# Performance work log

Hardware: AMD Instinct MI355X
Metric: run time of the kernel (lower is better)

## Reference

```python
import jax, jax.numpy as jnp
import numpy as np

N = 50000   # nodes
E = 800000  # edges
F = 128     # input features
W = 128     # hidden width
K = 5       # Chebyshev order


def setup_inputs() -> dict:
    key = jax.random.key(0)
    ks = jax.random.split(key, 12)
    x = jax.random.normal(ks[0], (N, F), jnp.float32)
    edge_index = jax.random.randint(ks[1], (2, E), 0, N, jnp.int32)
    def p(i, shape):
        return jax.random.normal(ks[i], shape, jnp.float32) * 0.05
    return {
        'x': x,
        'edge_index': edge_index,
        'W0': p(2, (K, F, W)), 'b0': p(3, (W,)),
        'W1': p(4, (K, W, W)), 'b1': p(5, (W,)),
        'W2': p(6, (K, W, W)), 'b2': p(7, (W,)),
        'Wl': p(8, (W, 1)),   'bl': p(9, (1,)),
    }


def _norm(edge_index):
    # PyG ChebConv norm with lambda_max=2.0, sym normalization:
    # Lhat = 2/lambda_max * (I - D^-1/2 A D^-1/2) - I  ->  diag 0, offdiag -d_r*d_c
    src, dst = edge_index[0], edge_index[1]
    ew = (src != dst).astype(jnp.float32)  # remove self loops
    deg = jax.ops.segment_sum(ew, src, num_segments=N)
    dinv = jnp.where(deg > 0, jax.lax.rsqrt(jnp.maximum(deg, 1.0)), 0.0)
    w = -ew * dinv[src] * dinv[dst]
    return src, dst, w


def _cheb_conv(h, Wk, b, src, dst, w):
    # Tx_0 = h; Tx_1 = Lhat h; Tx_k = 2 Lhat Tx_{k-1} - Tx_{k-2}
    def matvec(v):
        # gather from src, weight, scatter-add to dst: [E, C] message tensor
        return jax.ops.segment_sum(w[:, None] * v[src], dst, num_segments=N)
    Tx0 = h
    out = Tx0 @ Wk[0]
    Tx1 = matvec(Tx0)
    out = out + Tx1 @ Wk[1]
    for k in range(2, Wk.shape[0]):
        Tx2 = 2.0 * matvec(Tx1) - Tx0
        out = out + Tx2 @ Wk[k]
        Tx0, Tx1 = Tx1, Tx2
    return out + b


def reference(x, edge_index, W0, b0, W1, b1, W2, b2, Wl, bl):
    src, dst, w = _norm(edge_index)
    h = jax.nn.relu(_cheb_conv(x, W0, b0, src, dst, w))  # dropout = identity (eval)
    h = jax.nn.relu(_cheb_conv(h, W1, b1, src, dst, w))
    h = _cheb_conv(h, W2, b2, src, dst, w)
    return h @ Wl + bl  # [N, 1]
```

## Files before the change

kernel.cpp:

```cpp
#include <hip/hip_runtime.h>
#include <hip/hip_bf16.h>
#include <stdint.h>

#define N_NODES 50000
#define N_EDGES 800000
#define FEAT 128
#define CAP 64
#define NCVT 1600000
#define NTRW 163840
#define NPRE (NCVT + NTRW + N_EDGES)

typedef __attribute__((ext_vector_type(4))) float floatx4;
typedef __attribute__((ext_vector_type(8))) _Float16 half8;
typedef __attribute__((ext_vector_type(4))) _Float16 half4;

__device__ __forceinline__ float bf2f(unsigned short u) {
  union { unsigned u; float f; } v; v.u = ((unsigned)u) << 16; return v.f;
}
__device__ __forceinline__ unsigned short f2bf(float f) {
  union { float f; unsigned u; } v; v.f = f;
  unsigned r = v.u + 0x7fffu + ((v.u >> 16) & 1u);
  return (unsigned short)(r >> 16);
}
__device__ __forceinline__ unsigned pack_edge(float w, int s) {
  _Float16 h = (_Float16)w;
  unsigned short hb = __builtin_bit_cast(unsigned short, h);
  return ((unsigned)s << 16) | (unsigned)hb;
}
__device__ __forceinline__ float edge_w(unsigned e) {
  unsigned short hb = (unsigned short)(e & 0xFFFFu);
  return (float)__builtin_bit_cast(_Float16, hb);
}
__device__ __forceinline__ int edge_src(unsigned e) { return (int)(e >> 16); }

__global__ void k_pre1(const unsigned short* __restrict__ x,
                       const void* b0, const void* b1, const void* b2,
                       const void* wl, const void* bl,
                       float* __restrict__ pf, int* __restrict__ flag) {
  __shared__ int cnt_s;
  __shared__ int fl_s;
  int tid = threadIdx.x;
  if (tid == 0) cnt_s = 0;
  __syncthreads();
  int big = 0;
  for (int i = tid; i < 4096; i += 256) {
    unsigned short u = x[2 * i];
    int e = (u >> 7) & 0xFF;
    if (e >= 0xE0) big++;
  }
  atomicAdd(&cnt_s, big);
  __syncthreads();
  if (tid == 0) { fl_s = (cnt_s > 16) ? 1 : 0; flag[0] = fl_s; }
  __syncthreads();
  int fl = fl_s;
  for (int i = tid; i < 513; i += 256) {
    const void* src; int off;
    if (i < 128)      { src = b0; off = i; }
    else if (i < 256) { src = b1; off = i - 128; }
    else if (i < 384) { src = b2; off = i - 256; }
    else if (i < 512) { src = wl; off = i - 384; }
    else              { src = bl; off = 0; }
    pf[i] = fl ? ((const float*)src)[off] : bf2f(((const unsigned short*)src)[off]);
  }
}

__global__ void k_prev(const void* __restrict__ w2, float* __restrict__ pf,
                       const int* __restrict__ flag) {
  int d = blockIdx.x * 256 + threadIdx.x;
  if (d > 640) return;
  int fl = flag[0];
  if (d < 640) {
    int k = d >> 7, f = d & 127;
    float s = 0.f;
    const int base = (k << 14) + (f << 7);
    if (fl) {
      const float* w = (const float*)w2 + base;
#pragma unroll 8
      for (int i = 0; i < 128; ++i) s += w[i] * pf[384 + i];
    } else {
      const unsigned short* w = (const unsigned short*)w2 + base;
#pragma unroll 8
      for (int i = 0; i < 128; ++i) s += bf2f(w[i]) * pf[384 + i];
    }
    pf[520 + d] = s;
  } else {
    float s = 0.f;
    for (int i = 0; i < 128; ++i) s += pf[256 + i] * pf[384 + i];
    pf[1160] = s + pf[512];
  }
}

__global__ void k_pre2(const void* __restrict__ xp,
                       const void* __restrict__ w0, const void* __restrict__ w1,
                       const int* __restrict__ esrc, const int* __restrict__ edst,
                       _Float16* __restrict__ t0,
                       unsigned char* __restrict__ q0, float* __restrict__ s0,
                       _Float16* __restrict__ wt,
                       int* __restrict__ deg,
                       const int* __restrict__ flag) {
  int i = blockIdx.x * blockDim.x + threadIdx.x;
  int fl = flag[0];
  if (i < NCVT) {
    float4 o;
    if (fl) {
      o = ((const float4*)xp)[i];
    } else {
      ushort4 v = ((const ushort4*)xp)[i];
      o.x = bf2f(v.x); o.y = bf2f(v.y); o.z = bf2f(v.z); o.w = bf2f(v.w);
    }
    half4 h;
    h[0] = (_Float16)o.x; h[1] = (_Float16)o.y; h[2] = (_Float16)o.z; h[3] = (_Float16)o.w;
    ((half4*)t0)[i] = h;
    float mx = fmaxf(fmaxf(fabsf(o.x), fabsf(o.y)), fmaxf(fabsf(o.z), fabsf(o.w)));
#pragma unroll
    for (int d = 1; d < 32; d <<= 1) mx = fmaxf(mx, __shfl_xor(mx, d));
    float inv = mx > 0.f ? 127.f / mx : 0.f;
    int qa = (int)rintf(o.x * inv) + 128;
    int qb = (int)rintf(o.y * inv) + 128;
    int qc = (int)rintf(o.z * inv) + 128;
    int qd = (int)rintf(o.w * inv) + 128;
    ((unsigned*)q0)[i] = (unsigned)qa | ((unsigned)qb << 8) | ((unsigned)qc << 16) | ((unsigned)qd << 24);
    if ((i & 31) == 0) s0[i >> 5] = mx > 0.f ? mx / 127.f : 0.f;
  } else if (i < NCVT + NTRW) {
    int tid = i - NCVT;
    int li = tid >> 14;
    int r = tid & 16383;
    int n = r >> 7, kk = r & 127;
    int l = li / 5, k = li - l * 5;
    const void* w = (l == 0) ? w0 : w1;
    int idx = k * 16384 + kk * 128 + n;
    float v = fl ? ((const float*)w)[idx] : bf2f(((const unsigned short*)w)[idx]);
    wt[tid] = (_Float16)v;
  } else {
    int e = i - (NCVT + NTRW);
    if (e >= N_EDGES) return;
    int s = esrc[e], d = edst[e];
    if (s != d) atomicAdd(&deg[s], 1);
  }
}

__global__ void k_fill(const int* __restrict__ src, const int* __restrict__ dst,
                       const int* __restrict__ deg,
                       int* __restrict__ cnt, unsigned* __restrict__ edata) {
  int e = blockIdx.x * blockDim.x + threadIdx.x;
  if (e >= N_EDGES) return;
  int s = src[e], d = dst[e];
  if (s == d) return;
  int ds = deg[s], dd = deg[d];
  float w = (ds > 0 && dd > 0) ? -rsqrtf((float)ds) * rsqrtf((float)dd) : 0.f;
  int pos = atomicAdd(&cnt[d], 1);
  if (pos < CAP) edata[(d << 6) + pos] = pack_edge(w, s);
}

__global__ __launch_bounds__(256) void k_spmv(const unsigned* __restrict__ edata,
                                              const int* __restrict__ cnt,
                                              const unsigned char* __restrict__ Q,
                                              const float* __restrict__ S,
                                              const _Float16* __restrict__ Z,
                                              _Float16* __restrict__ Y,
                                              unsigned char* __restrict__ Qo,
                                              float* __restrict__ So,
                                              float alpha, int hasZ, int wshadow) {
  int wave = threadIdx.x >> 6, lane = threadIdx.x & 63;
  int q = lane >> 4, l16 = lane & 15;
  int node = blockIdx.x * 16 + wave * 4 + q;
  if (node >= N_NODES) return;
  int n_e = cnt[node]; if (n_e > CAP) n_e = CAP;
  int base = node << 6;

  float acc[8];
#pragma unroll
  for (int f = 0; f < 8; ++f) acc[f] = 0.f;
  float wsum = 0.f;

  unsigned e0 = (0 < n_e) ? edata[base + 0] : 0u;
  unsigned e1 = (1 < n_e) ? edata[base + 1] : 0u;
  unsigned e2 = (2 < n_e) ? edata[base + 2] : 0u;
  unsigned e3 = (3 < n_e) ? edata[base + 3] : 0u;
  unsigned e4 = (4 < n_e) ? edata[base + 4] : 0u;
  unsigned e5 = (5 < n_e) ? edata[base + 5] : 0u;
  unsigned e6 = (6 < n_e) ? edata[base + 6] : 0u;
  unsigned e7 = (7 < n_e) ? edata[base + 7] : 0u;
  uint2 r0 = ((const uint2*)(Q + (size_t)edge_src(e0) * FEAT))[l16];
  uint2 r1 = ((const uint2*)(Q + (size_t)edge_src(e1) * FEAT))[l16];
  uint2 r2 = ((const uint2*)(Q + (size_t)edge_src(e2) * FEAT))[l16];
  uint2 r3 = ((const uint2*)(Q + (size_t)edge_src(e3) * FEAT))[l16];
  float s0 = S[edge_src(e0)], s1 = S[edge_src(e1)], s2 = S[edge_src(e2)], s3 = S[edge_src(e3)];

  for (int j = 0; j < n_e; j += 4) {
    float ws0 = edge_w(e0) * s0, ws1 = edge_w(e1) * s1;
    float ws2 = edge_w(e2) * s2, ws3 = edge_w(e3) * s3;
    uint2 c0 = r0, c1 = r1, c2 = r2, c3 = r3;
    e0 = e4; e1 = e5; e2 = e6; e3 = e7;
    e4 = (j + 8 < n_e) ? edata[base + j + 8] : 0u;
    e5 = (j + 9 < n_e) ? edata[base + j + 9] : 0u;
    e6 = (j + 10 < n_e) ? edata[base + j + 10] : 0u;
    e7 = (j + 11 < n_e) ? edata[base + j + 11] : 0u;
    r0 = ((const uint2*)(Q + (size_t)edge_src(e0) * FEAT))[l16];
    r1 = ((const uint2*)(Q + (size_t)edge_src(e1) * FEAT))[l16];
    r2 = ((const uint2*)(Q + (size_t)edge_src(e2) * FEAT))[l16];
    r3 = ((const uint2*)(Q + (size_t)edge_src(e3) * FEAT))[l16];
    s0 = S[edge_src(e0)]; s1 = S[edge_src(e1)]; s2 = S[edge_src(e2)]; s3 = S[edge_src(e3)];
#define DEC8(c, w)                                                        \
    acc[0] = fmaf(w, (float)(c.x & 0xFFu), acc[0]);                       \
    acc[1] = fmaf(w, (float)((c.x >> 8) & 0xFFu), acc[1]);                \
    acc[2] = fmaf(w, (float)((c.x >> 16) & 0xFFu), acc[2]);               \
    acc[3] = fmaf(w, (float)(c.x >> 24), acc[3]);                         \
    acc[4] = fmaf(w, (float)(c.y & 0xFFu), acc[4]);                       \
    acc[5] = fmaf(w, (float)((c.y >> 8) & 0xFFu), acc[5]);                \
    acc[6] = fmaf(w, (float)((c.y >> 16) & 0xFFu), acc[6]);               \
    acc[7] = fmaf(w, (float)(c.y >> 24), acc[7]);
    DEC8(c0, ws0) DEC8(c1, ws1) DEC8(c2, ws2) DEC8(c3, ws3)
#undef DEC8
    wsum += (ws0 + ws1) + (ws2 + ws3);
  }
  float rx[8];
  float b128 = 128.f * wsum;
  if (hasZ) {
    half8 z = ((const half8*)(Z + (size_t)node * FEAT))[l16];
#pragma unroll
    for (int f = 0; f < 8; ++f) rx[f] = fmaf(alpha, acc[f] - b128, -(float)z[f]);
  } else {
#pragma unroll
    for (int f = 0; f < 8; ++f) rx[f] = alpha * (acc[f] - b128);
  }
  half8 res;
#pragma unroll
  for (int f = 0; f < 8; ++f) res[f] = (_Float16)rx[f];
  ((half8*)(Y + (size_t)node * FEAT))[l16] = res;
  if (wshadow) {
    float mx = 0.f;
#pragma unroll
    for (int f = 0; f < 8; ++f) mx = fmaxf(mx, fabsf(rx[f]));
#pragma unroll
    for (int o = 1; o < 16; o <<= 1) mx = fmaxf(mx, __shfl_xor(mx, o));
    float inv = mx > 0.f ? 127.f / mx : 0.f;
    int qb[8];
#pragma unroll
    for (int f = 0; f < 8; ++f) qb[f] = (int)rintf(rx[f] * inv) + 128;
    uint2 p;
    p.x = (unsigned)qb[0] | ((unsigned)qb[1] << 8) | ((unsigned)qb[2] << 16) | ((unsigned)qb[3] << 24);
    p.y = (unsigned)qb[4] | ((unsigned)qb[5] << 8) | ((unsigned)qb[6] << 16) | ((unsigned)qb[7] << 24);
    ((uint2*)(Qo + (size_t)node * FEAT))[l16] = p;
    if (l16 == 0) So[node] = mx > 0.f ? mx / 127.f : 0.f;
  }
}

__global__ __launch_bounds__(256) void k_smv(const unsigned* __restrict__ edata,
                                             const int* __restrict__ cnt,
                                             const float* __restrict__ h,
                                             const float* __restrict__ b,
                                             const float* __restrict__ bprev,
                                             float cL, float* __restrict__ y,
                                             int is_out, void* __restrict__ outp,
                                             const int* __restrict__ flag,
                                             const float* __restrict__ cptr) {
  int wave = threadIdx.x >> 6, lane = threadIdx.x & 63;
  int q = lane >> 4, l16 = lane & 15;
  int node = blockIdx.x * 16 + wave * 4 + q;
  if (node >= N_NODES) return;
  int n_e = cnt[node]; if (n_e > CAP) n_e = CAP;
  int base = node << 6;
  float s = 0.f;
  for (int j = l16; j < n_e; j += 16) {
    unsigned e = edata[base + j];
    s = fmaf(edge_w(e), b[edge_src(e)], s);
  }
#pragma unroll
  for (int o = 1; o < 16; o <<= 1) s += __shfl_xor(s, o);
  if (l16 == 0) {
    float r = fmaf(cL, s, h[node]) - (bprev ? bprev[node] : 0.f);
    if (!is_out) {
      y[node] = r;
    } else {
      r += cptr[0];
      if (flag[0]) ((float*)outp)[node] = r;
      else ((unsigned short*)outp)[node] = f2bf(r);
    }
  }
}

__global__ __launch_bounds__(256) void k_gemm(const _Float16* __restrict__ t0, const _Float16* __restrict__ t1,
                                              const _Float16* __restrict__ t2, const _Float16* __restrict__ t3,
                                              const _Float16* __restrict__ t4,
                                              const _Float16* __restrict__ wt,
                                              const float* __restrict__ bias,
                                              _Float16* __restrict__ dst, int mode,
                                              const float* __restrict__ v0,
                                              float* __restrict__ hout,
                                              unsigned char* __restrict__ q8,
                                              float* __restrict__ sc) {
  __shared__ _Float16 lb[128 * 136];
  const _Float16* tp[5] = {t0, t1, t2, t3, t4};
  int tid = threadIdx.x, wave = tid >> 6, lane = tid & 63;
  int quad = lane >> 4, l16 = lane & 15;
  int m0 = blockIdx.x * 128;
  floatx4 acc[2][8];
#pragma unroll
  for (int s = 0; s < 2; ++s)
#pragma unroll
    for (int j = 0; j < 8; ++j) acc[s][j] = (floatx4){0.f, 0.f, 0.f, 0.f};
  int arow[2];
  bool aval[2];
#pragma unroll
  for (int s = 0; s < 2; ++s) {
    arow[s] = m0 + wave * 32 + s * 16 + l16;
    aval[s] = arow[s] < N_NODES;
  }

#pragma unroll
  for (int k = 0; k < 5; ++k) {
    __syncthreads();
    {
      int n = tid >> 1, half = tid & 1;
      const uint4* sp = (const uint4*)(wt + k * 16384 + n * 128 + half * 64);
      uint4* dq = (uint4*)(lb + n * 136 + half * 64);
#pragma unroll
      for (int i = 0; i < 8; ++i) dq[i] = sp[i];
    }
    __syncthreads();
    const _Float16* A = tp[k];
#pragma unroll
    for (int ki = 0; ki < 4; ++ki) {
      half8 af[2];
#pragma unroll
      for (int s = 0; s < 2; ++s) {
        if (aval[s]) {
          af[s] = *((const half8*)(A + (size_t)arow[s] * FEAT + ki * 32 + quad * 8));
        } else {
#pragma unroll
          for (int i = 0; i < 8; ++i) af[s][i] = (_Float16)0.f;
        }
      }
#pragma unroll
      for (int j = 0; j < 8; ++j) {
        half8 bf = *((const half8*)(lb + (j * 16 + l16) * 136 + ki * 32 + quad * 8));
        acc[0][j] = __builtin_amdgcn_mfma_f32_16x16x32_f16(af[0], bf, acc[0][j], 0, 0, 0);
        acc[1][j] = __builtin_amdgcn_mfma_f32_16x16x32_f16(af[1], bf, acc[1][j], 0, 0, 0);
      }
    }
  }
#pragma unroll
  for (int s = 0; s < 2; ++s) {
    int rbase = m0 + wave * 32 + s * 16 + quad * 4;
    if (mode == 0) {
      float mx[4] = {0.f, 0.f, 0.f, 0.f};
#pragma unroll
      for (int j = 0; j < 8; ++j) {
        int col = j * 16 + l16;
        float b = bias[col];
#pragma unroll
        for (int r = 0; r < 4; ++r) {
          int m = rbase + r;
          float v = fmaxf(acc[s][j][r] + b, 0.f);
          if (m < N_NODES) dst[(size_t)m * FEAT + col] = (_Float16)v;
          mx[r] = fmaxf(mx[r], v);
        }
      }
#pragma unroll
      for (int o = 1; o < 16; o <<= 1) {
#pragma unroll
        for (int r = 0; r < 4; ++r) mx[r] = fmaxf(mx[r], __shfl_xor(mx[r], o));
      }
      float inv[4];
#pragma unroll
      for (int r = 0; r < 4; ++r) inv[r] = mx[r] > 0.f ? 127.f / mx[r] : 0.f;
      if (l16 == 0) {
#pragma unroll
        for (int r = 0; r < 4; ++r) {
          int m = rbase + r;
          if (m < N_NODES) sc[m] = mx[r] > 0.f ? mx[r] / 127.f : 0.f;
        }
      }
#pragma unroll
      for (int j = 0; j < 8; ++j) {
        int col = j * 16 + l16;
        float b = bias[col];
#pragma unroll
        for (int r = 0; r < 4; ++r) {
          int m = rbase + r;
          if (m < N_NODES) {
            float v = fmaxf(acc[s][j][r] + b, 0.f);
            int qv = (int)rintf(v * inv[r]) + 128;
            q8[(size_t)m * FEAT + col] = (unsigned char)qv;
          }
        }
      }
    } else {
      float p[5][4];
#pragma unroll
      for (int k = 0; k < 5; ++k)
#pragma unroll
        for (int r = 0; r < 4; ++r) p[k][r] = 0.f;
#pragma unroll
      for (int j = 0; j < 8; ++j) {
        int col = j * 16 + l16;
        float b = bias[col];
        float vv[5];
#pragma unroll
        for (int k = 0; k < 5; ++k) vv[k] = v0[k * 128 + col];
#pragma unroll
        for (int r = 0; r < 4; ++r) {
          float val = fmaxf(acc[s][j][r] + b, 0.f);
#pragma unroll
          for (int k = 0; k < 5; ++k) p[k][r] = fmaf(val, vv[k], p[k][r]);
        }
      }
#pragma unroll
      for (int o = 1; o < 16; o <<= 1) {
#pragma unroll
        for (int k = 0; k < 5; ++k)
#pragma unroll
          for (int r = 0; r < 4; ++r) p[k][r] += __shfl_xor(p[k][r], o);
      }
      if (l16 == 0) {
#pragma unroll
        for (int r = 0; r < 4; ++r) {
          int m = rbase + r;
          if (m < N_NODES) {
#pragma unroll
            for (int k = 0; k < 5; ++k) hout[k * N_NODES + m] = p[k][r];
          }
        }
      }
    }
  }
}

extern "C" void kernel_launch(void* const* d_in, const int* in_sizes, int n_in,
                              void* d_out, int out_size, void* d_ws, size_t ws_size,
                              hipStream_t stream) {
  const void* x  = d_in[0];
  const int* ei  = (const int*)d_in[1];
  const void* w0 = d_in[2];
  const void* b0 = d_in[3];
  const void* w1 = d_in[4];
  const void* b1 = d_in[5];
  const void* w2 = d_in[6];
  const void* b2 = d_in[7];
  const void* wl = d_in[8];
  const void* bl = d_in[9];
  const int* src = ei;
  const int* dst = ei + N_EDGES;

  char* ws = (char*)d_ws;
  size_t off = 0;
  auto alloc = [&](size_t bytes) -> char* {
    char* p = ws + off;
    off += (bytes + 255) & ~(size_t)255;
    return p;
  };
  _Float16* T[5];
  for (int i = 0; i < 5; ++i) T[i] = (_Float16*)alloc(sizeof(_Float16) * N_NODES * FEAT);
  unsigned char* Q[5];
  for (int i = 0; i < 5; ++i) Q[i] = (unsigned char*)alloc((size_t)N_NODES * FEAT);
  float* S[5];
  for (int i = 0; i < 5; ++i) S[i] = (float*)alloc(sizeof(float) * N_NODES);
  unsigned* edata = (unsigned*)alloc(sizeof(unsigned) * N_NODES * CAP);
  int* cnt = (int*)alloc(sizeof(int) * N_NODES * 2);
  int* deg = cnt + N_NODES;
  _Float16* wt = (_Float16*)alloc(sizeof(_Float16) * NTRW);
  float* pf = (float*)alloc(sizeof(float) * 1536);
  float* hbuf = (float*)alloc(sizeof(float) * 5 * N_NODES);
  float* bbuf = (float*)alloc(sizeof(float) * 3 * N_NODES);
  int* flag = (int*)alloc(sizeof(int));

  hipMemsetAsync(cnt, 0, sizeof(int) * N_NODES * 2, stream);
  k_pre1<<<1, 256, 0, stream>>>((const unsigned short*)x, b0, b1, b2, wl, bl, pf, flag);
  k_prev<<<3, 256, 0, stream>>>(w2, pf, flag);
  k_pre2<<<(NPRE + 255) / 256, 256, 0, stream>>>(x, w0, w1, src, dst, T[0], Q[0], S[0], wt, deg, flag);
  k_fill<<<(N_EDGES + 255) / 256, 256, 0, stream>>>(src, dst, deg, cnt, edata);

  int nblk_spmv = (N_NODES + 15) / 16;
  int nblk_gemm = (N_NODES + 127) / 128;
  const float* v = pf + 520;
  const float* cc = pf + 1160;

  for (int l = 0; l < 2; ++l) {
    k_spmv<<<nblk_spmv, 256, 0, stream>>>(edata, cnt, Q[0], S[0], nullptr, T[1], Q[1], S[1], 1.f, 0, 1);
    k_spmv<<<nblk_spmv, 256, 0, stream>>>(edata, cnt, Q[1], S[1], T[0], T[2], Q[2], S[2], 2.f, 1, 1);
    k_spmv<<<nblk_spmv, 256, 0, stream>>>(edata, cnt, Q[2], S[2], T[1], T[3], Q[3], S[3], 2.f, 1, 1);
    k_spmv<<<nblk_spmv, 256, 0, stream>>>(edata, cnt, Q[3], S[3], T[2], T[4], nullptr, nullptr, 2.f, 1, 0);
    k_gemm<<<nblk_gemm, 256, 0, stream>>>(T[0], T[1], T[2], T[3], T[4],
                                          wt + l * 5 * 16384, pf + l * 128, T[0],
                                          l, v, hbuf, Q[0], S[0]);
  }
  float* h0 = hbuf;
  float* h1 = hbuf + N_NODES;
  float* h2 = hbuf + 2 * N_NODES;
  float* h3 = hbuf + 3 * N_NODES;
  float* h4 = hbuf + 4 * N_NODES;
  float* b3 = bbuf;
  float* b2c = bbuf + N_NODES;
  float* b1c = bbuf + 2 * N_NODES;
  k_smv<<<nblk_spmv, 256, 0, stream>>>(edata, cnt, h3, h4, nullptr, 2.f, b3, 0, nullptr, flag, nullptr);
  k_smv<<<nblk_spmv, 256, 0, stream>>>(edata, cnt, h2, b3, h4, 2.f, b2c, 0, nullptr, flag, nullptr);
  k_smv<<<nblk_spmv, 256, 0, stream>>>(edata, cnt, h1, b2c, b3, 2.f, b1c, 0, nullptr, flag, nullptr);
  k_smv<<<nblk_spmv, 256, 0, stream>>>(edata, cnt, h0, b1c, b2c, 1.f, nullptr, 1, d_out, flag, cc);
}
```

Before: 449.9 us.

## Fuse edge fill and weight precompute into preprocessing; store 16-bit edge sources

Folds the k_fill and k_prev kernels into k_pre2, which removes two launches and one pass over the edge list. Degree counting and CSR-style bucket filling now happen in the same edge pass. Edge weights are no longer stored: the bucket keeps only a 16-bit source index, and the spmv/smv kernels rebuild the normalisation from deg (rsqrt of the source degree per edge, times the destination scale at the end). The input streams in preprocessing also switch to nontemporal loads and stores. The cost of this is an extra random gather of deg per edge in every propagation kernel, in exchange for half-size edge data.

```diff
diff --git a/kernel.cpp b/kernel.cpp
--- a/kernel.cpp
+++ b/kernel.cpp
@@ -8,11 +8,13 @@
 #define CAP 64
 #define NCVT 1600000
 #define NTRW 163840
-#define NPRE (NCVT + NTRW + N_EDGES)
+#define NPREV 768
+#define NPRE2 (NCVT + NTRW + N_EDGES + NPREV)
 
 typedef __attribute__((ext_vector_type(4))) float floatx4;
 typedef __attribute__((ext_vector_type(8))) _Float16 half8;
 typedef __attribute__((ext_vector_type(4))) _Float16 half4;
+typedef __attribute__((ext_vector_type(4))) unsigned short ushortx4;
 
 __device__ __forceinline__ float bf2f(unsigned short u) {
   union { unsigned u; float f; } v; v.u = ((unsigned)u) << 16; return v.f;
@@ -22,16 +24,6 @@
   unsigned r = v.u + 0x7fffu + ((v.u >> 16) & 1u);
   return (unsigned short)(r >> 16);
 }
-__device__ __forceinline__ unsigned pack_edge(float w, int s) {
-  _Float16 h = (_Float16)w;
-  unsigned short hb = __builtin_bit_cast(unsigned short, h);
-  return ((unsigned)s << 16) | (unsigned)hb;
-}
-__device__ __forceinline__ float edge_w(unsigned e) {
-  unsigned short hb = (unsigned short)(e & 0xFFFFu);
-  return (float)__builtin_bit_cast(_Float16, hb);
-}
-__device__ __forceinline__ int edge_src(unsigned e) { return (int)(e >> 16); }
 
 __global__ void k_pre1(const unsigned short* __restrict__ x,
                        const void* b0, const void* b1, const void* b2,
@@ -64,53 +56,30 @@
   }
 }
 
-__global__ void k_prev(const void* __restrict__ w2, float* __restrict__ pf,
-                       const int* __restrict__ flag) {
-  int d = blockIdx.x * 256 + threadIdx.x;
-  if (d > 640) return;
-  int fl = flag[0];
-  if (d < 640) {
-    int k = d >> 7, f = d & 127;
-    float s = 0.f;
-    const int base = (k << 14) + (f << 7);
-    if (fl) {
-      const float* w = (const float*)w2 + base;
-#pragma unroll 8
-      for (int i = 0; i < 128; ++i) s += w[i] * pf[384 + i];
-    } else {
-      const unsigned short* w = (const unsigned short*)w2 + base;
-#pragma unroll 8
-      for (int i = 0; i < 128; ++i) s += bf2f(w[i]) * pf[384 + i];
-    }
-    pf[520 + d] = s;
-  } else {
-    float s = 0.f;
-    for (int i = 0; i < 128; ++i) s += pf[256 + i] * pf[384 + i];
-    pf[1160] = s + pf[512];
-  }
-}
-
 __global__ void k_pre2(const void* __restrict__ xp,
                        const void* __restrict__ w0, const void* __restrict__ w1,
+                       const void* __restrict__ w2,
                        const int* __restrict__ esrc, const int* __restrict__ edst,
                        _Float16* __restrict__ t0,
                        unsigned char* __restrict__ q0, float* __restrict__ s0,
                        _Float16* __restrict__ wt,
-                       int* __restrict__ deg,
+                       int* __restrict__ deg, int* __restrict__ cnt,
+                       unsigned short* __restrict__ edata,
+                       float* __restrict__ pf,
                        const int* __restrict__ flag) {
   int i = blockIdx.x * blockDim.x + threadIdx.x;
-  int fl = flag[0];
   if (i < NCVT) {
-    float4 o;
+    int fl = flag[0];
+    floatx4 o;
     if (fl) {
-      o = ((const float4*)xp)[i];
+      o = __builtin_nontemporal_load((const floatx4*)xp + i);
     } else {
-      ushort4 v = ((const ushort4*)xp)[i];
+      ushortx4 v = __builtin_nontemporal_load((const ushortx4*)xp + i);
       o.x = bf2f(v.x); o.y = bf2f(v.y); o.z = bf2f(v.z); o.w = bf2f(v.w);
     }
     half4 h;
     h[0] = (_Float16)o.x; h[1] = (_Float16)o.y; h[2] = (_Float16)o.z; h[3] = (_Float16)o.w;
-    ((half4*)t0)[i] = h;
+    __builtin_nontemporal_store(h, (half4*)t0 + i);
     float mx = fmaxf(fmaxf(fabsf(o.x), fabsf(o.y)), fmaxf(fabsf(o.z), fabsf(o.w)));
 #pragma unroll
     for (int d = 1; d < 32; d <<= 1) mx = fmaxf(mx, __shfl_xor(mx, d));
@@ -119,9 +88,11 @@
     int qb = (int)rintf(o.y * inv) + 128;
     int qc = (int)rintf(o.z * inv) + 128;
     int qd = (int)rintf(o.w * inv) + 128;
-    ((unsigned*)q0)[i] = (unsigned)qa | ((unsigned)qb << 8) | ((unsigned)qc << 16) | ((unsigned)qd << 24);
+    unsigned pk = (unsigned)qa | ((unsigned)qb << 8) | ((unsigned)qc << 16) | ((unsigned)qd << 24);
+    __builtin_nontemporal_store(pk, (unsigned*)q0 + i);
     if ((i & 31) == 0) s0[i >> 5] = mx > 0.f ? mx / 127.f : 0.f;
   } else if (i < NCVT + NTRW) {
+    int fl = flag[0];
     int tid = i - NCVT;
     int li = tid >> 14;
     int r = tid & 16383;
@@ -131,29 +102,44 @@
     int idx = k * 16384 + kk * 128 + n;
     float v = fl ? ((const float*)w)[idx] : bf2f(((const unsigned short*)w)[idx]);
     wt[tid] = (_Float16)v;
+  } else if (i < NCVT + NTRW + N_EDGES) {
+    int e = i - (NCVT + NTRW);
+    int s = __builtin_nontemporal_load(esrc + e);
+    int d = __builtin_nontemporal_load(edst + e);
+    if (s == d) return;
+    atomicAdd(&deg[s], 1);
+    int pos = atomicAdd(&cnt[d], 1);
+    if (pos < CAP) edata[((size_t)d << 6) + pos] = (unsigned short)s;
   } else {
-    int e = i - (NCVT + NTRW);
-    if (e >= N_EDGES) return;
-    int s = esrc[e], d = edst[e];
-    if (s != d) atomicAdd(&deg[s], 1);
-  }
-}
-
-__global__ void k_fill(const int* __restrict__ src, const int* __restrict__ dst,
-                       const int* __restrict__ deg,
-                       int* __restrict__ cnt, unsigned* __restrict__ edata) {
-  int e = blockIdx.x * blockDim.x + threadIdx.x;
-  if (e >= N_EDGES) return;
-  int s = src[e], d = dst[e];
-  if (s == d) return;
-  int ds = deg[s], dd = deg[d];
-  float w = (ds > 0 && dd > 0) ? -rsqrtf((float)ds) * rsqrtf((float)dd) : 0.f;
-  int pos = atomicAdd(&cnt[d], 1);
-  if (pos < CAP) edata[(d << 6) + pos] = pack_edge(w, s);
-}
-
-__global__ __launch_bounds__(256) void k_spmv(const unsigned* __restrict__ edata,
+    int t = i - (NCVT + NTRW + N_EDGES);
+    if (t > 640) return;
+    int fl = flag[0];
+    if (t < 640) {
+      int k = t >> 7, f = t & 127;
+      float s = 0.f;
+      const int base = (k << 14) + (f << 7);
+      if (fl) {
+        const float* w = (const float*)w2 + base;
+#pragma unroll 8
+        for (int q = 0; q < 128; ++q) s += w[q] * pf[384 + q];
+      } else {
+        const unsigned short* w = (const unsigned short*)w2 + base;
+#pragma unroll 8
+        for (int q = 0; q < 128; ++q) s += bf2f(w[q]) * pf[384 + q];
+      }
+      pf[520 + t] = s;
+    } else {
+      float s = 0.f;
+      for (int q = 0; q < 128; ++q) s += pf[256 + q] * pf[384 + q];
+      pf[1160] = s + pf[512];
+    }
+  }
+}
+
+
+__global__ __launch_bounds__(256) void k_spmv(const unsigned short* __restrict__ edata,
                                               const int* __restrict__ cnt,
+                                              const int* __restrict__ deg,
                                               const unsigned char* __restrict__ Q,
                                               const float* __restrict__ S,
                                               const _Float16* __restrict__ Z,
@@ -166,41 +152,40 @@
   int node = blockIdx.x * 16 + wave * 4 + q;
   if (node >= N_NODES) return;
   int n_e = cnt[node]; if (n_e > CAP) n_e = CAP;
-  int base = node << 6;
+  const unsigned short* ed = edata + ((size_t)node << 6);
 
   float acc[8];
 #pragma unroll
   for (int f = 0; f < 8; ++f) acc[f] = 0.f;
   float wsum = 0.f;
 
-  unsigned e0 = (0 < n_e) ? edata[base + 0] : 0u;
-  unsigned e1 = (1 < n_e) ? edata[base + 1] : 0u;
-  unsigned e2 = (2 < n_e) ? edata[base + 2] : 0u;
-  unsigned e3 = (3 < n_e) ? edata[base + 3] : 0u;
-  unsigned e4 = (4 < n_e) ? edata[base + 4] : 0u;
-  unsigned e5 = (5 < n_e) ? edata[base + 5] : 0u;
-  unsigned e6 = (6 < n_e) ? edata[base + 6] : 0u;
-  unsigned e7 = (7 < n_e) ? edata[base + 7] : 0u;
-  uint2 r0 = ((const uint2*)(Q + (size_t)edge_src(e0) * FEAT))[l16];
-  uint2 r1 = ((const uint2*)(Q + (size_t)edge_src(e1) * FEAT))[l16];
-  uint2 r2 = ((const uint2*)(Q + (size_t)edge_src(e2) * FEAT))[l16];
-  uint2 r3 = ((const uint2*)(Q + (size_t)edge_src(e3) * FEAT))[l16];
-  float s0 = S[edge_src(e0)], s1 = S[edge_src(e1)], s2 = S[edge_src(e2)], s3 = S[edge_src(e3)];
+#define LOADE(t, sv, wv)                                  \
+  if ((t) < n_e) {                                        \
+    int _s = (int)ed[(t)];                                \
+    sv = _s;                                              \
+    wv = rsqrtf((float)deg[_s]) * S[_s];                  \
+  } else { sv = 0; wv = 0.f; }
+
+  int s0, s1, s2, s3, s4, s5, s6, s7;
+  float w0, w1, w2, w3, w4, w5, w6, w7;
+  LOADE(0, s0, w0) LOADE(1, s1, w1) LOADE(2, s2, w2) LOADE(3, s3, w3)
+  LOADE(4, s4, w4) LOADE(5, s5, w5) LOADE(6, s6, w6) LOADE(7, s7, w7)
+  uint2 r0 = ((const uint2*)(Q + (size_t)s0 * FEAT))[l16];
+  uint2 r1 = ((const uint2*)(Q + (size_t)s1 * FEAT))[l16];
+  uint2 r2 = ((const uint2*)(Q + (size_t)s2 * FEAT))[l16];
+  uint2 r3 = ((const uint2*)(Q + (size_t)s3 * FEAT))[l16];
 
   for (int j = 0; j < n_e; j += 4) {
-    float ws0 = edge_w(e0) * s0, ws1 = edge_w(e1) * s1;
-    float ws2 = edge_w(e2) * s2, ws3 = edge_w(e3) * s3;
+    float ws0 = w0, ws1 = w1, ws2 = w2, ws3 = w3;
     uint2 c0 = r0, c1 = r1, c2 = r2, c3 = r3;
-    e0 = e4; e1 = e5; e2 = e6; e3 = e7;
-    e4 = (j + 8 < n_e) ? edata[base + j + 8] : 0u;
-    e5 = (j + 9 < n_e) ? edata[base + j + 9] : 0u;
-    e6 = (j + 10 < n_e) ? edata[base + j + 10] : 0u;
-    e7 = (j + 11 < n_e) ? edata[base + j + 11] : 0u;
-    r0 = ((const uint2*)(Q + (size_t)edge_src(e0) * FEAT))[l16];
-    r1 = ((const uint2*)(Q + (size_t)edge_src(e1) * FEAT))[l16];
-    r2 = ((const uint2*)(Q + (size_t)edge_src(e2) * FEAT))[l16];
-    r3 = ((const uint2*)(Q + (size_t)edge_src(e3) * FEAT))[l16];
-    s0 = S[edge_src(e0)]; s1 = S[edge_src(e1)]; s2 = S[edge_src(e2)]; s3 = S[edge_src(e3)];
+    s0 = s4; s1 = s5; s2 = s6; s3 = s7;
+    w0 = w4; w1 = w5; w2 = w6; w3 = w7;
+    LOADE(j + 8, s4, w4) LOADE(j + 9, s5, w5)
+    LOADE(j + 10, s6, w6) LOADE(j + 11, s7, w7)
+    r0 = ((const uint2*)(Q + (size_t)s0 * FEAT))[l16];
+    r1 = ((const uint2*)(Q + (size_t)s1 * FEAT))[l16];
+    r2 = ((const uint2*)(Q + (size_t)s2 * FEAT))[l16];
+    r3 = ((const uint2*)(Q + (size_t)s3 * FEAT))[l16];
 #define DEC8(c, w)                                                        \
     acc[0] = fmaf(w, (float)(c.x & 0xFFu), acc[0]);                       \
     acc[1] = fmaf(w, (float)((c.x >> 8) & 0xFFu), acc[1]);                \
@@ -214,15 +199,19 @@
 #undef DEC8
     wsum += (ws0 + ws1) + (ws2 + ws3);
   }
+#undef LOADE
+  int dn = deg[node];
+  float dvn = dn > 0 ? rsqrtf((float)dn) : 0.f;
+  float m = -alpha * dvn;
   float rx[8];
   float b128 = 128.f * wsum;
   if (hasZ) {
     half8 z = ((const half8*)(Z + (size_t)node * FEAT))[l16];
 #pragma unroll
-    for (int f = 0; f < 8; ++f) rx[f] = fmaf(alpha, acc[f] - b128, -(float)z[f]);
+    for (int f = 0; f < 8; ++f) rx[f] = fmaf(m, acc[f] - b128, -(float)z[f]);
   } else {
 #pragma unroll
-    for (int f = 0; f < 8; ++f) rx[f] = alpha * (acc[f] - b128);
+    for (int f = 0; f < 8; ++f) rx[f] = m * (acc[f] - b128);
   }
   half8 res;
 #pragma unroll
@@ -246,8 +235,9 @@
   }
 }
 
-__global__ __launch_bounds__(256) void k_smv(const unsigned* __restrict__ edata,
+__global__ __launch_bounds__(256) void k_smv(const unsigned short* __restrict__ edata,
                                              const int* __restrict__ cnt,
+                                             const int* __restrict__ deg,
                                              const float* __restrict__ h,
                                              const float* __restrict__ b,
                                              const float* __restrict__ bprev,
@@ -260,16 +250,18 @@
   int node = blockIdx.x * 16 + wave * 4 + q;
   if (node >= N_NODES) return;
   int n_e = cnt[node]; if (n_e > CAP) n_e = CAP;
-  int base = node << 6;
+  const unsigned short* ed = edata + ((size_t)node << 6);
   float s = 0.f;
   for (int j = l16; j < n_e; j += 16) {
-    unsigned e = edata[base + j];
-    s = fmaf(edge_w(e), b[edge_src(e)], s);
+    int sc = (int)ed[j];
+    s = fmaf(rsqrtf((float)deg[sc]), b[sc], s);
   }
 #pragma unroll
   for (int o = 1; o < 16; o <<= 1) s += __shfl_xor(s, o);
   if (l16 == 0) {
-    float r = fmaf(cL, s, h[node]) - (bprev ? bprev[node] : 0.f);
+    int dn = deg[node];
+    float dvn = dn > 0 ? rsqrtf((float)dn) : 0.f;
+    float r = fmaf(-cL * dvn, s, h[node]) - (bprev ? bprev[node] : 0.f);
     if (!is_out) {
       y[node] = r;
     } else {
@@ -456,7 +448,7 @@
   for (int i = 0; i < 5; ++i) Q[i] = (unsigned char*)alloc((size_t)N_NODES * FEAT);
   float* S[5];
   for (int i = 0; i < 5; ++i) S[i] = (float*)alloc(sizeof(float) * N_NODES);
-  unsigned* edata = (unsigned*)alloc(sizeof(unsigned) * N_NODES * CAP);
+  unsigned short* edata = (unsigned short*)alloc(sizeof(unsigned short) * N_NODES * CAP);
   int* cnt = (int*)alloc(sizeof(int) * N_NODES * 2);
   int* deg = cnt + N_NODES;
   _Float16* wt = (_Float16*)alloc(sizeof(_Float16) * NTRW);
@@ -467,9 +459,8 @@
 
   hipMemsetAsync(cnt, 0, sizeof(int) * N_NODES * 2, stream);
   k_pre1<<<1, 256, 0, stream>>>((const unsigned short*)x, b0, b1, b2, wl, bl, pf, flag);
-  k_prev<<<3, 256, 0, stream>>>(w2, pf, flag);
-  k_pre2<<<(NPRE + 255) / 256, 256, 0, stream>>>(x, w0, w1, src, dst, T[0], Q[0], S[0], wt, deg, flag);
-  k_fill<<<(N_EDGES + 255) / 256, 256, 0, stream>>>(src, dst, deg, cnt, edata);
+  k_pre2<<<NPRE2 / 256, 256, 0, stream>>>(x, w0, w1, w2, src, dst, T[0], Q[0], S[0], wt,
+                                          deg, cnt, edata, pf, flag);
 
   int nblk_spmv = (N_NODES + 15) / 16;
   int nblk_gemm = (N_NODES + 127) / 128;
@@ -477,10 +468,10 @@
   const float* cc = pf + 1160;
 
   for (int l = 0; l < 2; ++l) {
-    k_spmv<<<nblk_spmv, 256, 0, stream>>>(edata, cnt, Q[0], S[0], nullptr, T[1], Q[1], S[1], 1.f, 0, 1);
-    k_spmv<<<nblk_spmv, 256, 0, stream>>>(edata, cnt, Q[1], S[1], T[0], T[2], Q[2], S[2], 2.f, 1, 1);
-    k_spmv<<<nblk_spmv, 256, 0, stream>>>(edata, cnt, Q[2], S[2], T[1], T[3], Q[3], S[3], 2.f, 1, 1);
-    k_spmv<<<nblk_spmv, 256, 0, stream>>>(edata, cnt, Q[3], S[3], T[2], T[4], nullptr, nullptr, 2.f, 1, 0);
+    k_spmv<<<nblk_spmv, 256, 0, stream>>>(edata, cnt, deg, Q[0], S[0], nullptr, T[1], Q[1], S[1], 1.f, 0, 1);
+    k_spmv<<<nblk_spmv, 256, 0, stream>>>(edata, cnt, deg, Q[1], S[1], T[0], T[2], Q[2], S[2], 2.f, 1, 1);
+    k_spmv<<<nblk_spmv, 256, 0, stream>>>(edata, cnt, deg, Q[2], S[2], T[1], T[3], Q[3], S[3], 2.f, 1, 1);
+    k_spmv<<<nblk_spmv, 256, 0, stream>>>(edata, cnt, deg, Q[3], S[3], T[2], T[4], nullptr, nullptr, 2.f, 1, 0);
     k_gemm<<<nblk_gemm, 256, 0, stream>>>(T[0], T[1], T[2], T[3], T[4],
                                           wt + l * 5 * 16384, pf + l * 128, T[0],
                                           l, v, hbuf, Q[0], S[0]);
@@ -493,8 +484,8 @@
   float* b3 = bbuf;
   float* b2c = bbuf + N_NODES;
   float* b1c = bbuf + 2 * N_NODES;
-  k_smv<<<nblk_spmv, 256, 0, stream>>>(edata, cnt, h3, h4, nullptr, 2.f, b3, 0, nullptr, flag, nullptr);
-  k_smv<<<nblk_spmv, 256, 0, stream>>>(edata, cnt, h2, b3, h4, 2.f, b2c, 0, nullptr, flag, nullptr);
-  k_smv<<<nblk_spmv, 256, 0, stream>>>(edata, cnt, h1, b2c, b3, 2.f, b1c, 0, nullptr, flag, nullptr);
-  k_smv<<<nblk_spmv, 256, 0, stream>>>(edata, cnt, h0, b1c, b2c, 1.f, nullptr, 1, d_out, flag, cc);
-}
+  k_smv<<<nblk_spmv, 256, 0, stream>>>(edata, cnt, deg, h3, h4, nullptr, 2.f, b3, 0, nullptr, flag, nullptr);
+  k_smv<<<nblk_spmv, 256, 0, stream>>>(edata, cnt, deg, h2, b3, h4, 2.f, b2c, 0, nullptr, flag, nullptr);
+  k_smv<<<nblk_spmv, 256, 0, stream>>>(edata, cnt, deg, h1, b2c, b3, 2.f, b1c, 0, nullptr, flag, nullptr);
+  k_smv<<<nblk_spmv, 256, 0, stream>>>(edata, cnt, deg, h0, b1c, b2c, 1.f, nullptr, 1, d_out, flag, cc);
+}
```

After: 628.9 us. +39.8%, slower.

## Fuse preprocessing passes and defer edge weight packing to a dense pass

Applied to the files above, without the earlier changes.

Merges k_prev, the degree count and the edge bucketing into one k_pre2 launch whose blocks interleave edge work with feature conversion. Edges are bucketed by destination with only 16-bit source ids, so the bucketing no longer has to wait for degrees. A new dense k_wpack pass then computes normalized weights and writes the packed edge array with zero padding. This drops one kernel launch and one full read of the edge lists, and adds an extra 6.4 MB intermediate buffer plus a full rewrite of the padded edge table.

```diff
diff --git a/kernel.cpp b/kernel.cpp
--- a/kernel.cpp
+++ b/kernel.cpp
@@ -7,12 +7,16 @@
 #define FEAT 128
 #define CAP 64
 #define NCVT 1600000
-#define NTRW 163840
-#define NPRE (NCVT + NTRW + N_EDGES)
+
+#define B_CONV 6250
+#define B_TRW  640
+#define B_EDGE 3125
+#define B_TOT  10018
 
 typedef __attribute__((ext_vector_type(4))) float floatx4;
 typedef __attribute__((ext_vector_type(8))) _Float16 half8;
 typedef __attribute__((ext_vector_type(4))) _Float16 half4;
+typedef __attribute__((ext_vector_type(4))) unsigned short ushortx4;
 
 __device__ __forceinline__ float bf2f(unsigned short u) {
   union { unsigned u; float f; } v; v.u = ((unsigned)u) << 16; return v.f;
@@ -64,92 +68,112 @@
   }
 }
 
-__global__ void k_prev(const void* __restrict__ w2, float* __restrict__ pf,
-                       const int* __restrict__ flag) {
-  int d = blockIdx.x * 256 + threadIdx.x;
-  if (d > 640) return;
-  int fl = flag[0];
-  if (d < 640) {
-    int k = d >> 7, f = d & 127;
-    float s = 0.f;
-    const int base = (k << 14) + (f << 7);
-    if (fl) {
-      const float* w = (const float*)w2 + base;
-#pragma unroll 8
-      for (int i = 0; i < 128; ++i) s += w[i] * pf[384 + i];
-    } else {
-      const unsigned short* w = (const unsigned short*)w2 + base;
-#pragma unroll 8
-      for (int i = 0; i < 128; ++i) s += bf2f(w[i]) * pf[384 + i];
-    }
-    pf[520 + d] = s;
-  } else {
-    float s = 0.f;
-    for (int i = 0; i < 128; ++i) s += pf[256 + i] * pf[384 + i];
-    pf[1160] = s + pf[512];
-  }
-}
-
 __global__ void k_pre2(const void* __restrict__ xp,
                        const void* __restrict__ w0, const void* __restrict__ w1,
+                       const void* __restrict__ w2,
                        const int* __restrict__ esrc, const int* __restrict__ edst,
                        _Float16* __restrict__ t0,
                        unsigned char* __restrict__ q0, float* __restrict__ s0,
                        _Float16* __restrict__ wt,
-                       int* __restrict__ deg,
+                       int* __restrict__ deg, int* __restrict__ cnt,
+                       unsigned short* __restrict__ edata16,
+                       float* __restrict__ pf,
                        const int* __restrict__ flag) {
-  int i = blockIdx.x * blockDim.x + threadIdx.x;
-  int fl = flag[0];
-  if (i < NCVT) {
-    float4 o;
+  int b = blockIdx.x, tid = threadIdx.x;
+  int o;
+  if (b < 10000) {
+    int g = b >> 4, r = b & 15;
+    if (r < 5) {
+      int e = (g * 5 + r) * 256 + tid;
+      int s = __builtin_nontemporal_load(esrc + e);
+      int d = __builtin_nontemporal_load(edst + e);
+      if (s == d) return;
+      atomicAdd(&deg[s], 1);
+      int pos = atomicAdd(&cnt[d], 1);
+      if (pos < CAP) edata16[((size_t)d << 6) + pos] = (unsigned short)s;
+      return;
+    }
+    o = g * 11 + (r - 5);
+  } else {
+    o = 6875 + (b - 10000);
+  }
+  if (o < B_CONV) {
+    int i = o * 256 + tid;
+    int fl = flag[0];
+    floatx4 v;
     if (fl) {
-      o = ((const float4*)xp)[i];
+      v = __builtin_nontemporal_load((const floatx4*)xp + i);
     } else {
-      ushort4 v = ((const ushort4*)xp)[i];
-      o.x = bf2f(v.x); o.y = bf2f(v.y); o.z = bf2f(v.z); o.w = bf2f(v.w);
+      ushortx4 u = __builtin_nontemporal_load((const ushortx4*)xp + i);
+      v.x = bf2f(u.x); v.y = bf2f(u.y); v.z = bf2f(u.z); v.w = bf2f(u.w);
     }
     half4 h;
-    h[0] = (_Float16)o.x; h[1] = (_Float16)o.y; h[2] = (_Float16)o.z; h[3] = (_Float16)o.w;
+    h[0] = (_Float16)v.x; h[1] = (_Float16)v.y; h[2] = (_Float16)v.z; h[3] = (_Float16)v.w;
     ((half4*)t0)[i] = h;
-    float mx = fmaxf(fmaxf(fabsf(o.x), fabsf(o.y)), fmaxf(fabsf(o.z), fabsf(o.w)));
+    float mx = fmaxf(fmaxf(fabsf(v.x), fabsf(v.y)), fmaxf(fabsf(v.z), fabsf(v.w)));
 #pragma unroll
     for (int d = 1; d < 32; d <<= 1) mx = fmaxf(mx, __shfl_xor(mx, d));
     float inv = mx > 0.f ? 127.f / mx : 0.f;
-    int qa = (int)rintf(o.x * inv) + 128;
-    int qb = (int)rintf(o.y * inv) + 128;
-    int qc = (int)rintf(o.z * inv) + 128;
-    int qd = (int)rintf(o.w * inv) + 128;
+    int qa = (int)rintf(v.x * inv) + 128;
+    int qb = (int)rintf(v.y * inv) + 128;
+    int qc = (int)rintf(v.z * inv) + 128;
+    int qd = (int)rintf(v.w * inv) + 128;
     ((unsigned*)q0)[i] = (unsigned)qa | ((unsigned)qb << 8) | ((unsigned)qc << 16) | ((unsigned)qd << 24);
     if ((i & 31) == 0) s0[i >> 5] = mx > 0.f ? mx / 127.f : 0.f;
-  } else if (i < NCVT + NTRW) {
-    int tid = i - NCVT;
-    int li = tid >> 14;
-    int r = tid & 16383;
+  } else if (o < B_CONV + B_TRW) {
+    int t = (o - B_CONV) * 256 + tid;
+    int fl = flag[0];
+    int li = t >> 14;
+    int r = t & 16383;
     int n = r >> 7, kk = r & 127;
     int l = li / 5, k = li - l * 5;
     const void* w = (l == 0) ? w0 : w1;
     int idx = k * 16384 + kk * 128 + n;
     float v = fl ? ((const float*)w)[idx] : bf2f(((const unsigned short*)w)[idx]);
-    wt[tid] = (_Float16)v;
+    wt[t] = (_Float16)v;
   } else {
-    int e = i - (NCVT + NTRW);
-    if (e >= N_EDGES) return;
-    int s = esrc[e], d = edst[e];
-    if (s != d) atomicAdd(&deg[s], 1);
-  }
-}
-
-__global__ void k_fill(const int* __restrict__ src, const int* __restrict__ dst,
-                       const int* __restrict__ deg,
-                       int* __restrict__ cnt, unsigned* __restrict__ edata) {
-  int e = blockIdx.x * blockDim.x + threadIdx.x;
-  if (e >= N_EDGES) return;
-  int s = src[e], d = dst[e];
-  if (s == d) return;
-  int ds = deg[s], dd = deg[d];
-  float w = (ds > 0 && dd > 0) ? -rsqrtf((float)ds) * rsqrtf((float)dd) : 0.f;
-  int pos = atomicAdd(&cnt[d], 1);
-  if (pos < CAP) edata[(d << 6) + pos] = pack_edge(w, s);
+    int t = (o - B_CONV - B_TRW) * 256 + tid;
+    if (t > 640) return;
+    int fl = flag[0];
+    if (t < 640) {
+      int k = t >> 7, f = t & 127;
+      float s = 0.f;
+      const int base = (k << 14) + (f << 7);
+      if (fl) {
+        const float* w = (const float*)w2 + base;
+#pragma unroll 8
+        for (int q = 0; q < 128; ++q) s += w[q] * pf[384 + q];
+      } else {
+        const unsigned short* w = (const unsigned short*)w2 + base;
+#pragma unroll 8
+        for (int q = 0; q < 128; ++q) s += bf2f(w[q]) * pf[384 + q];
+      }
+      pf[520 + t] = s;
+    } else {
+      float s = 0.f;
+      for (int q = 0; q < 128; ++q) s += pf[256 + q] * pf[384 + q];
+      pf[1160] = s + pf[512];
+    }
+  }
+}
+
+__global__ __launch_bounds__(256) void k_wpack(const unsigned short* __restrict__ ed16,
+                                               const int* __restrict__ cnt,
+                                               const int* __restrict__ deg,
+                                               unsigned* __restrict__ edata) {
+  int t = blockIdx.x * 256 + threadIdx.x;
+  int node = t >> 6, slot = t & 63;
+  if (node >= N_NODES) return;
+  int n_e = cnt[node]; if (n_e > CAP) n_e = CAP;
+  unsigned out = 0u;
+  if (slot < n_e) {
+    int s = (int)ed16[t];
+    int dd = deg[node];
+    int ds = deg[s];
+    float w = (ds > 0 && dd > 0) ? -rsqrtf((float)ds) * rsqrtf((float)dd) : 0.f;
+    out = pack_edge(w, s);
+  }
+  edata[t] = out;
 }
 
 __global__ __launch_bounds__(256) void k_spmv(const unsigned* __restrict__ edata,
@@ -457,9 +481,10 @@
   float* S[5];
   for (int i = 0; i < 5; ++i) S[i] = (float*)alloc(sizeof(float) * N_NODES);
   unsigned* edata = (unsigned*)alloc(sizeof(unsigned) * N_NODES * CAP);
+  unsigned short* edata16 = (unsigned short*)alloc(sizeof(unsigned short) * N_NODES * CAP);
   int* cnt = (int*)alloc(sizeof(int) * N_NODES * 2);
   int* deg = cnt + N_NODES;
-  _Float16* wt = (_Float16*)alloc(sizeof(_Float16) * NTRW);
+  _Float16* wt = (_Float16*)alloc(sizeof(_Float16) * 163840);
   float* pf = (float*)alloc(sizeof(float) * 1536);
   float* hbuf = (float*)alloc(sizeof(float) * 5 * N_NODES);
   float* bbuf = (float*)alloc(sizeof(float) * 3 * N_NODES);
@@ -467,9 +492,9 @@
 
   hipMemsetAsync(cnt, 0, sizeof(int) * N_NODES * 2, stream);
   k_pre1<<<1, 256, 0, stream>>>((const unsigned short*)x, b0, b1, b2, wl, bl, pf, flag);
-  k_prev<<<3, 256, 0, stream>>>(w2, pf, flag);
-  k_pre2<<<(NPRE + 255) / 256, 256, 0, stream>>>(x, w0, w1, src, dst, T[0], Q[0], S[0], wt, deg, flag);
-  k_fill<<<(N_EDGES + 255) / 256, 256, 0, stream>>>(src, dst, deg, cnt, edata);
+  k_pre2<<<B_TOT, 256, 0, stream>>>(x, w0, w1, w2, src, dst, T[0], Q[0], S[0], wt,
+                                    deg, cnt, edata16, pf, flag);
+  k_wpack<<<(N_NODES * CAP) / 256, 256, 0, stream>>>(edata16, cnt, deg, edata);
 
   int nblk_spmv = (N_NODES + 15) / 16;
   int nblk_gemm = (N_NODES + 127) / 128;
```

After: 455.8 us. About the same (+1.3%).
